# Kernel tuning notes

Hardware: AMD Instinct MI355X
Metric: run time of the kernel (lower is better)

## Reference

```python
import jax, jax.numpy as jnp
import numpy as np

H, D = 8, 16
F = H * D              # hidden_dim = 128
L = 2                  # num HGT layers
NS = [50000, 20000, 10000]                     # gene, disease, drug node counts
EDGE_META = [(0, 0), (0, 1), (2, 0), (2, 1)]   # (src_type, dst_type) per edge type
ES = [300000, 150000, 100000, 50000]
OFFS = [0, NS[0], NS[0] + NS[1], NS[0] + NS[1] + NS[2]]
NTOT = OFFS[-1]
R, T = len(EDGE_META), len(NS)
SQRT_D = float(np.sqrt(D))


def setup_inputs() -> dict:
    key = jax.random.key(0)
    ks = jax.random.split(key, 32)
    inp = {}
    inp["x_gene"] = jax.random.normal(ks[0], (NS[0], F), jnp.float32)
    inp["x_disease"] = jax.random.normal(ks[1], (NS[1], F), jnp.float32)
    inp["x_drug"] = jax.random.normal(ks[2], (NS[2], F), jnp.float32)
    inp["Wkqv"] = 0.05 * jax.random.normal(ks[3], (L, T, F, 3 * F), jnp.float32)
    inp["bkqv"] = jnp.zeros((L, T, 3 * F), jnp.float32)
    inp["Ak"] = 0.1 * jax.random.normal(ks[4], (L, R, H, D, D), jnp.float32)
    inp["Av"] = 0.1 * jax.random.normal(ks[5], (L, R, H, D, D), jnp.float32)
    inp["prel"] = jnp.ones((L, R, H), jnp.float32)   # PyG inits p_rel to ones
    inp["Wout"] = 0.05 * jax.random.normal(ks[6], (L, T, F, F), jnp.float32)
    inp["bout"] = jnp.zeros((L, T, F), jnp.float32)
    inp["skip"] = jnp.ones((L, T), jnp.float32)      # PyG inits skip to 1
    names = ["ei_gg", "ei_gd", "ei_rg", "ei_rd"]
    for i, (name, (st, dt), E) in enumerate(zip(names, EDGE_META, ES)):
        src = jax.random.randint(ks[10 + 2 * i], (E,), 0, NS[st], dtype=jnp.int32)
        dst = jax.random.randint(ks[11 + 2 * i], (E,), 0, NS[dt], dtype=jnp.int32)
        inp[name] = jnp.stack([src, dst])
    return inp


def _hgt_layer(xs, eis, Wkqv_l, bkqv_l, Ak_l, Av_l, prel_l, Wout_l, bout_l, skip_l):
    """One PyG-style HGTConv layer over the heterogeneous graph."""
    kqv = [x @ Wkqv_l[t] + bkqv_l[t] for t, x in enumerate(xs)]
    k = [a[:, :F].reshape(-1, H, D) for a in kqv]
    q = [a[:, F:2 * F].reshape(-1, H, D) for a in kqv]
    v = [a[:, 2 * F:].reshape(-1, H, D) for a in kqv]

    alphas, dsts, ves = [], [], []
    for r, (st, dt) in enumerate(EDGE_META):
        src, dst = eis[r][0], eis[r][1]
        # relation-specific per-head transforms applied on source node set
        k_r = jnp.einsum('nhd,hde->nhe', k[st], Ak_l[r])
        v_r = jnp.einsum('nhd,hde->nhe', v[st], Av_l[r])
        ke = k_r[src]                      # [E, H, D]
        ve = v_r[src]                      # [E, H, D]
        qe = q[dt][dst]                    # [E, H, D]
        a = (qe * ke).sum(-1) * prel_l[r] / SQRT_D   # [E, H]
        alphas.append(a)
        dsts.append(dst + OFFS[dt])
        ves.append(ve)
    alpha = jnp.concatenate(alphas, 0)     # [Etot, H]
    dstg = jnp.concatenate(dsts, 0)        # [Etot]
    ve = jnp.concatenate(ves, 0)           # [Etot, H, D]

    # segment softmax over all incoming edges per destination node
    amax = jax.ops.segment_max(alpha, dstg, num_segments=NTOT)
    ex = jnp.exp(alpha - amax[dstg])
    denom = jax.ops.segment_sum(ex, dstg, num_segments=NTOT)
    w = ex / denom[dstg]
    out = jax.ops.segment_sum(ve * w[..., None], dstg, num_segments=NTOT)
    out = out.reshape(NTOT, F)

    new_xs = []
    for t, x in enumerate(xs):
        o_t = out[OFFS[t]:OFFS[t + 1]]
        o = jax.nn.gelu(o_t, approximate=False) @ Wout_l[t] + bout_l[t]
        a_s = jax.nn.sigmoid(skip_l[t])
        new_xs.append(a_s * o + (1.0 - a_s) * x)
    return new_xs


def reference(x_gene, x_disease, x_drug, Wkqv, bkqv, Ak, Av, prel, Wout, bout,
              skip, ei_gg, ei_gd, ei_rg, ei_rd):
    xs = [x_gene, x_disease, x_drug]
    eis = [ei_gg, ei_gd, ei_rg, ei_rd]
    for l in range(L):
        new = _hgt_layer(xs, eis, Wkqv[l], bkqv[l], Ak[l], Av[l], prel[l],
                         Wout[l], bout[l], skip[l])
        # encoder: dropout(relu(conv_out)) + residual; dropout = identity (eval)
        xs = [jax.nn.relu(n) + x for n, x in zip(new, xs)]
    return tuple(xs)
```

## Files before the change

kernel.cpp:

```cpp
#include <hip/hip_runtime.h>


#define NTOT  80000
#define ETOT  600000
#define NSRC  120000
#define SLOTS 128

typedef unsigned short u16;
typedef unsigned int   u32;
typedef __attribute__((ext_vector_type(8))) short short8;
typedef __attribute__((ext_vector_type(4))) float f32x4;

__device__ __forceinline__ u16 f2bf(float f){
  union { float f; u32 i; } v; v.f = f;
  u32 x = v.i;
  return (u16)((x + 0x7fffu + ((x >> 16) & 1u)) >> 16);
}
__device__ __forceinline__ void unp4(uint4 a, float* o){
  union { u32 i; float f; } t;
  t.i = a.x << 16;        o[0]=t.f;  t.i = a.x & 0xffff0000u; o[1]=t.f;
  t.i = a.y << 16;        o[2]=t.f;  t.i = a.y & 0xffff0000u; o[3]=t.f;
  t.i = a.z << 16;        o[4]=t.f;  t.i = a.z & 0xffff0000u; o[5]=t.f;
  t.i = a.w << 16;        o[6]=t.f;  t.i = a.w & 0xffff0000u; o[7]=t.f;
}
__device__ __forceinline__ void load16bf(const u16* p, float* o){
  unp4(*(const uint4*)p, o); unp4(*(const uint4*)(p + 8), o + 8);
}


#define PR0 2560000
#define PR1 (PR0 + 8*32768)
#define PR2 (PR1 + 2*6*16384)
#define PR3 (PR2 + 2048)
#define PR4 (PR3 + ETOT)

__global__ __launch_bounds__(256) void prep_all(
    const float* __restrict__ xg, const float* __restrict__ xd,
    const float* __restrict__ xr, float* __restrict__ X, u16* __restrict__ Xbf,
    const float* __restrict__ Wkqv, const float* __restrict__ bkqv,
    const float* __restrict__ Ak, const float* __restrict__ Av,
    const float* __restrict__ Wout,
    u16* __restrict__ WeffT, u16* __restrict__ WqT, u16* __restrict__ WoutT,
    float* __restrict__ beff,
    const int* __restrict__ e0, const int* __restrict__ e1,
    const int* __restrict__ e2, const int* __restrict__ e3,
    int* __restrict__ cnt, int* __restrict__ elist)
{
  int i = blockIdx.x * 256 + threadIdx.x;
  if (i < PR0){
    const float* src; int off;
    if (i < 1600000)      { src = xg; off = i; }
    else if (i < 2240000) { src = xd; off = i - 1600000; }
    else                  { src = xr; off = i - 2240000; }
    float4 v = ((const float4*)src)[off];
    ((float4*)X)[i] = v;
    uint2 b;
    b.x = (u32)f2bf(v.x) | ((u32)f2bf(v.y) << 16);
    b.y = (u32)f2bf(v.z) | ((u32)f2bf(v.w) << 16);
    ((uint2*)Xbf)[i] = b;
    return;
  }
  if (i < PR1){
    int j = i - PR0;
    int lr = j >> 15, rem = j & 32767, n = rem >> 7, k = rem & 127;
    int l = lr >> 2, r = lr & 3;
    int st = (r >= 2) ? 2 : 0;
    const float* W = Wkqv + (size_t)(l*3 + st) * 49152;
    float acc = 0.f;
    if (n < 128){
      int h = n >> 4, e = n & 15;
      const float* Am = Ak + (size_t)(l*4 + r) * 2048 + h*256;
#pragma unroll
      for (int d = 0; d < 16; d++) acc += W[k*384 + h*16 + d] * Am[d*16 + e];
    } else {
      int n2 = n - 128, h = n2 >> 4, e = n2 & 15;
      const float* Am = Av + (size_t)(l*4 + r) * 2048 + h*256;
#pragma unroll
      for (int d = 0; d < 16; d++) acc += W[k*384 + 256 + h*16 + d] * Am[d*16 + e];
    }
    WeffT[j] = f2bf(acc);
    return;
  }
  if (i < PR2){
    int j = i - PR1;
    if (j < 6*16384){
      int lt = j >> 14, rem = j & 16383, n = rem >> 7, k = rem & 127;
      WqT[j] = f2bf(Wkqv[(size_t)lt*49152 + k*384 + 128 + n]);
    } else {
      int j2 = j - 6*16384;
      int lt = j2 >> 14, rem = j2 & 16383, n = rem >> 7, k = rem & 127;
      WoutT[j2] = f2bf(Wout[(size_t)lt*16384 + k*128 + n]);
    }
    return;
  }
  if (i < PR3){
    int m = i - PR2;
    int lr = m >> 8, jj = m & 255;
    int l = lr >> 2, r = lr & 3;
    int st = (r >= 2) ? 2 : 0;
    const float* b = bkqv + (size_t)(l*3 + st) * 384;
    float acc = 0.f;
    if (jj < 128){
      int h = jj >> 4, e = jj & 15;
      const float* Am = Ak + (size_t)(l*4 + r) * 2048 + h*256;
#pragma unroll
      for (int d = 0; d < 16; d++) acc += b[h*16 + d] * Am[d*16 + e];
    } else {
      int j2 = jj - 128, h = j2 >> 4, e = j2 & 15;
      const float* Am = Av + (size_t)(l*4 + r) * 2048 + h*256;
#pragma unroll
      for (int d = 0; d < 16; d++) acc += b[256 + h*16 + d] * Am[d*16 + e];
    }
    beff[lr * 256 + jj] = acc;
    return;
  }
  if (i < PR4){
    int e = i - PR3;
    const int* ei; int E, loc, offd, rnoff, rel;
    if (e < 300000)      { ei = e0; E = 300000; loc = e;          offd = 0;     rnoff = 0;      rel = 0; }
    else if (e < 450000) { ei = e1; E = 150000; loc = e - 300000; offd = 50000; rnoff = 50000;  rel = 1; }
    else if (e < 550000) { ei = e2; E = 100000; loc = e - 450000; offd = 0;     rnoff = 100000; rel = 2; }
    else                 { ei = e3; E = 50000;  loc = e - 550000; offd = 50000; rnoff = 110000; rel = 3; }
    int src = ei[loc], dst = ei[E + loc];
    int dstg = offd + dst;
    int pos = atomicAdd(&cnt[dstg], 1);
    if (pos < SLOTS) elist[dstg*SLOTS + pos] = ((rnoff + src) << 2) | rel;
  }
}


__device__ __forceinline__ void stage_bt(const u16* __restrict__ src, u16* BTl){
  int tid = threadIdx.x;
  const uint4* g = (const uint4*)src;
  uint4 tmp[8];
#pragma unroll
  for (int i = 0; i < 8; i++) tmp[i] = g[tid + i*256];
#pragma unroll
  for (int i = 0; i < 8; i++){
    int L = (tid + i*256) * 16;
    int Ls = L ^ (((L >> 8) & 7) << 4);
    *(uint4*)((char*)BTl + Ls) = tmp[i];
  }
}

__device__ __forceinline__ void gemm_core16(
    const u16* __restrict__ A, const u16* BTl, int M, int bm,
    f32x4 acc[8])
{
  int tid = threadIdx.x;
  int lane = tid & 63, w = tid >> 6;
  int quad = lane >> 4, lm = lane & 15;
  int row = bm + w*16 + lm;
  short8 af[4];
  if (row < M){
    const u16* ap = A + (size_t)row*128 + quad*8;
#pragma unroll
    for (int c = 0; c < 4; c++) af[c] = *(const short8*)(ap + c*32);
  } else {
    short8 z = {0,0,0,0,0,0,0,0};
#pragma unroll
    for (int c = 0; c < 4; c++) af[c] = z;
  }
#pragma unroll
  for (int nt = 0; nt < 8; nt++) acc[nt] = (f32x4){0.f,0.f,0.f,0.f};
#pragma unroll
  for (int nt = 0; nt < 8; nt++){
    int rowb = nt*16 + lm;
    int base = rowb*256 + quad*16;
    int sw = (rowb & 7) << 4;
#pragma unroll
    for (int c = 0; c < 4; c++){
      short8 bf = *(const short8*)((const char*)BTl + ((base + c*64) ^ sw));
      acc[nt] = __builtin_amdgcn_mfma_f32_16x16x32_bf16(af[c], bf, acc[nt], 0, 0, 0);
    }
  }
}

__global__ __launch_bounds__(256) void mfma_gemm_qkv(
    const u16* __restrict__ Xbf,
    const u16* __restrict__ WqTl, const float* __restrict__ bl,
    const u16* __restrict__ WeffTl, const float* __restrict__ beffl,
    u16* __restrict__ qg, u16* __restrict__ kv)
{
  __shared__ u16 BTl[16384];
  int by = blockIdx.x;
  const u16* A; const u16* BT; const float* bias;
  u16* C; int ldc, bm, M, bn;
  if (by < 1252){
    int t, roff;
    if (by < 782)       { t = 0; bm = by*64;         M = 50000; roff = 0; }
    else if (by < 1095) { t = 1; bm = (by-782)*64;   M = 20000; roff = 50000; }
    else                { t = 2; bm = (by-1095)*64;  M = 10000; roff = 70000; }
    A = Xbf + (size_t)roff*128;
    BT = WqTl + (size_t)t*16384;
    bias = bl + (size_t)t*384 + 128;
    C = qg + (size_t)roff*128; ldc = 128; bn = 0;
  } else {
    int idx = by - 1252;
    bn = (idx < 1878) ? 0 : 128;
    int tile = (idx < 1878) ? idx : idx - 1878;
    int r, soff, ooff;
    if (tile < 782)       { r = 0; bm = tile*64;        M = 50000; soff = 0;     ooff = 0; }
    else if (tile < 1564) { r = 1; bm = (tile-782)*64;  M = 50000; soff = 0;     ooff = 50000; }
    else if (tile < 1721) { r = 2; bm = (tile-1564)*64; M = 10000; soff = 70000; ooff = 100000; }
    else                  { r = 3; bm = (tile-1721)*64; M = 10000; soff = 70000; ooff = 110000; }
    A = Xbf + (size_t)soff*128;
    BT = WeffTl + (size_t)r*32768 + (size_t)bn*128;
    bias = beffl + (size_t)r*256 + bn;
    C = kv + (size_t)ooff*256 + bn; ldc = 256;
  }
  stage_bt(BT, BTl);
  __syncthreads();
  f32x4 acc[8];
  gemm_core16(A, BTl, M, bm, acc);
  int lane = threadIdx.x & 63, w = threadIdx.x >> 6;
  int quad = lane >> 4, lm = lane & 15;
#pragma unroll
  for (int nt = 0; nt < 8; nt++){
    int col = nt*16 + lm;
    float bb = bias[col];
#pragma unroll
    for (int i = 0; i < 4; i++){
      int r = bm + w*16 + quad*4 + i;
      if (r < M) C[(size_t)r*ldc + col] = f2bf(acc[nt][i] + bb);
    }
  }
}


__global__ __launch_bounds__(256) void attn_out(
    const u16* __restrict__ qg,
    const u16* __restrict__ kv,
    const float* __restrict__ prel,
    const int* __restrict__ cnt,
    const int* __restrict__ elist,
    const u16* __restrict__ WoutTl,
    const float* __restrict__ bl,
    const float* __restrict__ skipl,
    float* __restrict__ Xall, u16* __restrict__ Xbfall)
{
  __shared__ u16 BT[16384];
  __shared__ u16 G[2048];
  int bid = blockIdx.x;
  int t, bm, roff;
  if (bid < 3125)      { t = 0; bm = bid*16;        roff = 0; }
  else if (bid < 4375) { t = 1; bm = (bid-3125)*16; roff = 50000; }
  else                 { t = 2; bm = (bid-4375)*16; roff = 70000; }

  stage_bt(WoutTl + (size_t)t*16384, BT);

  int tid = threadIdx.x;
  int slot = tid >> 4;
  int n = roff + bm + slot;
  int lane = tid & 63;
  int sub = (lane >> 3) & 1;
  int h = lane & 7;
  float sc0 = prel[0*8+h]*0.25f, sc1 = prel[1*8+h]*0.25f,
        sc2 = prel[2*8+h]*0.25f, sc3 = prel[3*8+h]*0.25f;
  float q[16];
  load16bf(qg + (size_t)n * 128 + h*16, q);
  float acc[16] = {};
  float dsum = 0.f;
  int start = n * SLOTS, c = cnt[n];
  if (c > SLOTS) c = SLOTS;

  auto edge = [&](int ev, uint4 ka, uint4 kb, uint4 va, uint4 vb){
    float ke[16], ve[16];
    unp4(ka, ke); unp4(kb, ke + 8);
    unp4(va, ve); unp4(vb, ve + 8);
    float a = 0.f;
#pragma unroll
    for (int d = 0; d < 16; d++) a += q[d] * ke[d];
    int r = ev & 3;
    float s = (r == 0) ? sc0 : (r == 1) ? sc1 : (r == 2) ? sc2 : sc3;
    float ex = expf(a * s);
    dsum += ex;
#pragma unroll
    for (int d = 0; d < 16; d++) acc[d] += ex * ve[d];
  };

  int idx = sub;
#pragma unroll 1
  for (; idx + 6 < c; idx += 8){
    int e0 = elist[start + idx + 0], e1 = elist[start + idx + 2],
        e2 = elist[start + idx + 4], e3 = elist[start + idx + 6];
    const u16* p0 = kv + (size_t)(e0 >> 2) * 256 + h*16;
    const u16* p1 = kv + (size_t)(e1 >> 2) * 256 + h*16;
    const u16* p2 = kv + (size_t)(e2 >> 2) * 256 + h*16;
    const u16* p3 = kv + (size_t)(e3 >> 2) * 256 + h*16;
    uint4 k0a = *(const uint4*)p0,         k0b = *(const uint4*)(p0 + 8);
    uint4 k1a = *(const uint4*)p1,         k1b = *(const uint4*)(p1 + 8);
    uint4 k2a = *(const uint4*)p2,         k2b = *(const uint4*)(p2 + 8);
    uint4 k3a = *(const uint4*)p3,         k3b = *(const uint4*)(p3 + 8);
    uint4 v0a = *(const uint4*)(p0 + 128), v0b = *(const uint4*)(p0 + 136);
    uint4 v1a = *(const uint4*)(p1 + 128), v1b = *(const uint4*)(p1 + 136);
    uint4 v2a = *(const uint4*)(p2 + 128), v2b = *(const uint4*)(p2 + 136);
    uint4 v3a = *(const uint4*)(p3 + 128), v3b = *(const uint4*)(p3 + 136);
    edge(e0, k0a, k0b, v0a, v0b);
    edge(e1, k1a, k1b, v1a, v1b);
    edge(e2, k2a, k2b, v2a, v2b);
    edge(e3, k3a, k3b, v3a, v3b);
  }
#pragma unroll 1
  for (; idx < c; idx += 2){
    int ev = elist[start + idx];
    const u16* p = kv + (size_t)(ev >> 2) * 256 + h*16;
    uint4 ka = *(const uint4*)p,         kb = *(const uint4*)(p + 8);
    uint4 va = *(const uint4*)(p + 128), vb = *(const uint4*)(p + 136);
    edge(ev, ka, kb, va, vb);
  }

  dsum += __shfl_xor(dsum, 8);
#pragma unroll
  for (int d = 0; d < 16; d++) acc[d] += __shfl_xor(acc[d], 8);

  if (sub == 0){
    float inv = (c > 0) ? 1.f / dsum : 0.f;
    u16 o[16];
#pragma unroll
    for (int d = 0; d < 16; d++){
      float x = acc[d] * inv;
      o[d] = f2bf(0.5f * x * (1.f + erff(x * 0.70710678118654752f)));
    }
    uint4 p0, p1;
    p0.x = o[0]|(o[1]<<16);   p0.y = o[2]|(o[3]<<16);
    p0.z = o[4]|(o[5]<<16);   p0.w = o[6]|(o[7]<<16);
    p1.x = o[8]|(o[9]<<16);   p1.y = o[10]|(o[11]<<16);
    p1.z = o[12]|(o[13]<<16); p1.w = o[14]|(o[15]<<16);
    int b0 = slot*256 + h*32;
    int sw = (slot & 7) << 4;
    *(uint4*)((char*)G + (b0 ^ sw))        = p0;
    *(uint4*)((char*)G + ((b0 + 16) ^ sw)) = p1;
  }
  __syncthreads();

  int w = tid >> 6;
  int quad = lane >> 4, lm = lane & 15;
  short8 af[4];
  {
    int base = lm*256 + quad*16;
    int sw = (lm & 7) << 4;
#pragma unroll
    for (int c2 = 0; c2 < 4; c2++)
      af[c2] = *(const short8*)((const char*)G + ((base + c2*64) ^ sw));
  }
  f32x4 oacc[2];
#pragma unroll
  for (int nt = 0; nt < 2; nt++){
    oacc[nt] = (f32x4){0.f,0.f,0.f,0.f};
    int rowb = w*32 + nt*16 + lm;
    int base = rowb*256 + quad*16;
    int sw = (rowb & 7) << 4;
#pragma unroll
    for (int c2 = 0; c2 < 4; c2++){
      short8 bf = *(const short8*)((const char*)BT + ((base + c2*64) ^ sw));
      oacc[nt] = __builtin_amdgcn_mfma_f32_16x16x32_bf16(af[c2], bf, oacc[nt], 0, 0, 0);
    }
  }
  float a_s = 1.f / (1.f + expf(-skipl[t]));
  float b_s = 1.f - a_s;
  const float* bias = bl + (size_t)t*128;
  float* X = Xall + (size_t)roff*128;
  u16* Xb = Xbfall ? (Xbfall + (size_t)roff*128) : (u16*)0;
#pragma unroll
  for (int nt = 0; nt < 2; nt++){
    int col = w*32 + nt*16 + lm;
    float bb = bias[col];
#pragma unroll
    for (int i = 0; i < 4; i++){
      int r = bm + quad*4 + i;
      float* xp = X + (size_t)r*128 + col;
      float x = *xp;
      float o = oacc[nt][i] + bb;
      float xn = fmaxf(a_s*o + b_s*x, 0.f) + x;
      *xp = xn;
      if (Xb) Xb[(size_t)r*128 + col] = f2bf(xn);
    }
  }
}


extern "C" void kernel_launch(void* const* d_in, const int* in_sizes, int n_in,
                              void* d_out, int out_size, void* d_ws, size_t ws_size,
                              hipStream_t stream)
{
  const float* xg   = (const float*)d_in[0];
  const float* xd   = (const float*)d_in[1];
  const float* xr_  = (const float*)d_in[2];
  const float* Wkqv = (const float*)d_in[3];
  const float* bkqv = (const float*)d_in[4];
  const float* Ak   = (const float*)d_in[5];
  const float* Av   = (const float*)d_in[6];
  const float* prel = (const float*)d_in[7];
  const float* Wout = (const float*)d_in[8];
  const float* bout = (const float*)d_in[9];
  const float* skip = (const float*)d_in[10];
  const int* ei[4] = {(const int*)d_in[11], (const int*)d_in[12],
                      (const int*)d_in[13], (const int*)d_in[14]};

  float* X = (float*)d_out;

  char* p = (char*)d_ws;
  auto alloc = [&](size_t b)->void*{ void* r = (void*)p; p += (b + 255) & ~(size_t)255; return r; };
  int*   cnt   = (int*)  alloc((size_t)NTOT * 4);
  int*   elist = (int*)  alloc((size_t)NTOT * SLOTS * 4);
  float* beff  = (float*)alloc((size_t)8 * 256 * 4);
  u16*   qg    = (u16*)  alloc((size_t)NTOT * 128 * 2);
  u16*   kv    = (u16*)  alloc((size_t)NSRC * 256 * 2);
  u16*   Xbf   = (u16*)  alloc((size_t)NTOT * 128 * 2);
  u16*   WqT   = (u16*)  alloc((size_t)6 * 16384 * 2);
  u16*   WeffT = (u16*)  alloc((size_t)8 * 32768 * 2);
  u16*   WoutT = (u16*)  alloc((size_t)6 * 16384 * 2);
  (void)ws_size; (void)in_sizes; (void)n_in; (void)out_size;

  hipMemsetAsync(cnt, 0, (size_t)NTOT * 4, stream);

  prep_all<<<(PR4 + 255)/256, 256, 0, stream>>>(
      xg, xd, xr_, X, Xbf,
      Wkqv, bkqv, Ak, Av, Wout, WeffT, WqT, WoutT, beff,
      ei[0], ei[1], ei[2], ei[3], cnt, elist);

  for (int l = 0; l < 2; l++){
    mfma_gemm_qkv<<<1252 + 3756, 256, 0, stream>>>(
        Xbf,
        WqT + (size_t)l*3*16384, bkqv + (size_t)l*3*384,
        WeffT + (size_t)l*4*32768, beff + (size_t)l*4*256,
        qg, kv);
    attn_out<<<5000, 256, 0, stream>>>(
        qg, kv, prel + l*32, cnt, elist,
        WoutT + (size_t)l*3*16384, bout + (size_t)l*3*128, skip + l*3,
        X, (l == 0) ? Xbf : (u16*)0);
  }
}
```

Measured before the change: 409.6 us.

## Reuse A fragments across Q and KV tiles; load Wout directly into registers

```diff
diff --git a/kernel.cpp b/kernel.cpp
--- a/kernel.cpp
+++ b/kernel.cpp
@@ -143,24 +143,16 @@
   }
 }
 
-__device__ __forceinline__ void gemm_core16(
-    const u16* __restrict__ A, const u16* BTl, int M, int bm,
-    f32x4 acc[8])
+__device__ __forceinline__ void do_tile(
+    const u16* __restrict__ BTsrc, const float* __restrict__ bias,
+    u16* __restrict__ C, int ldc, int bm, int M, const short8 af[4], u16* BTl)
 {
+  stage_bt(BTsrc, BTl);
+  __syncthreads();
   int tid = threadIdx.x;
   int lane = tid & 63, w = tid >> 6;
   int quad = lane >> 4, lm = lane & 15;
-  int row = bm + w*16 + lm;
-  short8 af[4];
-  if (row < M){
-    const u16* ap = A + (size_t)row*128 + quad*8;
-#pragma unroll
-    for (int c = 0; c < 4; c++) af[c] = *(const short8*)(ap + c*32);
-  } else {
-    short8 z = {0,0,0,0,0,0,0,0};
-#pragma unroll
-    for (int c = 0; c < 4; c++) af[c] = z;
-  }
+  f32x4 acc[8];
 #pragma unroll
   for (int nt = 0; nt < 8; nt++) acc[nt] = (f32x4){0.f,0.f,0.f,0.f};
 #pragma unroll
@@ -172,6 +164,17 @@
     for (int c = 0; c < 4; c++){
       short8 bf = *(const short8*)((const char*)BTl + ((base + c*64) ^ sw));
       acc[nt] = __builtin_amdgcn_mfma_f32_16x16x32_bf16(af[c], bf, acc[nt], 0, 0, 0);
+    }
+  }
+  __syncthreads();
+#pragma unroll
+  for (int nt = 0; nt < 8; nt++){
+    int col = nt*16 + lm;
+    float bb = bias[col];
+#pragma unroll
+    for (int i = 0; i < 4; i++){
+      int r = bm + w*16 + quad*4 + i;
+      if (r < M) C[(size_t)r*ldc + col] = f2bf(acc[nt][i] + bb);
     }
   }
 }
@@ -184,45 +187,37 @@
 {
   __shared__ u16 BTl[16384];
   int by = blockIdx.x;
-  const u16* A; const u16* BT; const float* bias;
-  u16* C; int ldc, bm, M, bn;
-  if (by < 1252){
-    int t, roff;
-    if (by < 782)       { t = 0; bm = by*64;         M = 50000; roff = 0; }
-    else if (by < 1095) { t = 1; bm = (by-782)*64;   M = 20000; roff = 50000; }
-    else                { t = 2; bm = (by-1095)*64;  M = 10000; roff = 70000; }
-    A = Xbf + (size_t)roff*128;
-    BT = WqTl + (size_t)t*16384;
-    bias = bl + (size_t)t*384 + 128;
-    C = qg + (size_t)roff*128; ldc = 128; bn = 0;
+  int t, bm, M, roff, rbase, o0, o1; bool haskv;
+  if (by < 782)      { t = 0; bm = by*64;        M = 50000; roff = 0;     haskv = true;  rbase = 0; o0 = 0;      o1 = 50000; }
+  else if (by < 939) { t = 2; bm = (by-782)*64;  M = 10000; roff = 70000; haskv = true;  rbase = 2; o0 = 100000; o1 = 110000; }
+  else               { t = 1; bm = (by-939)*64;  M = 20000; roff = 50000; haskv = false; rbase = 0; o0 = 0;      o1 = 0; }
+
+  int tid = threadIdx.x;
+  int lane = tid & 63, w = tid >> 6;
+  int quad = lane >> 4, lm = lane & 15;
+  int row = bm + w*16 + lm;
+  short8 af[4];
+  if (row < M){
+    const u16* ap = Xbf + (size_t)(roff + row)*128 + quad*8;
+#pragma unroll
+    for (int c = 0; c < 4; c++) af[c] = *(const short8*)(ap + c*32);
   } else {
-    int idx = by - 1252;
-    bn = (idx < 1878) ? 0 : 128;
-    int tile = (idx < 1878) ? idx : idx - 1878;
-    int r, soff, ooff;
-    if (tile < 782)       { r = 0; bm = tile*64;        M = 50000; soff = 0;     ooff = 0; }
-    else if (tile < 1564) { r = 1; bm = (tile-782)*64;  M = 50000; soff = 0;     ooff = 50000; }
-    else if (tile < 1721) { r = 2; bm = (tile-1564)*64; M = 10000; soff = 70000; ooff = 100000; }
-    else                  { r = 3; bm = (tile-1721)*64; M = 10000; soff = 70000; ooff = 110000; }
-    A = Xbf + (size_t)soff*128;
-    BT = WeffTl + (size_t)r*32768 + (size_t)bn*128;
-    bias = beffl + (size_t)r*256 + bn;
-    C = kv + (size_t)ooff*256 + bn; ldc = 256;
-  }
-  stage_bt(BT, BTl);
-  __syncthreads();
-  f32x4 acc[8];
-  gemm_core16(A, BTl, M, bm, acc);
-  int lane = threadIdx.x & 63, w = threadIdx.x >> 6;
-  int quad = lane >> 4, lm = lane & 15;
-#pragma unroll
-  for (int nt = 0; nt < 8; nt++){
-    int col = nt*16 + lm;
-    float bb = bias[col];
-#pragma unroll
-    for (int i = 0; i < 4; i++){
-      int r = bm + w*16 + quad*4 + i;
-      if (r < M) C[(size_t)r*ldc + col] = f2bf(acc[nt][i] + bb);
+    short8 z = {0,0,0,0,0,0,0,0};
+#pragma unroll
+    for (int c = 0; c < 4; c++) af[c] = z;
+  }
+
+  do_tile(WqTl + (size_t)t*16384, bl + (size_t)t*384 + 128,
+          qg + (size_t)roff*128, 128, bm, M, af, BTl);
+  if (haskv){
+#pragma unroll 1
+    for (int s = 0; s < 4; s++){
+      int r  = rbase + (s >> 1);
+      int bn = (s & 1) * 128;
+      int oo = (s < 2) ? o0 : o1;
+      do_tile(WeffTl + (size_t)r*32768 + (size_t)bn*128,
+              beffl + (size_t)r*256 + bn,
+              kv + (size_t)oo*256 + bn, 256, bm, M, af, BTl);
     }
   }
 }
@@ -239,15 +234,12 @@
     const float* __restrict__ skipl,
     float* __restrict__ Xall, u16* __restrict__ Xbfall)
 {
-  __shared__ u16 BT[16384];
   __shared__ u16 G[2048];
   int bid = blockIdx.x;
   int t, bm, roff;
   if (bid < 3125)      { t = 0; bm = bid*16;        roff = 0; }
   else if (bid < 4375) { t = 1; bm = (bid-3125)*16; roff = 50000; }
   else                 { t = 2; bm = (bid-4375)*16; roff = 70000; }
-
-  stage_bt(WoutTl + (size_t)t*16384, BT);
 
   int tid = threadIdx.x;
   int slot = tid >> 4;
@@ -310,6 +302,19 @@
     edge(ev, ka, kb, va, vb);
   }
 
+  int w = tid >> 6;
+  int quad = lane >> 4, lm = lane & 15;
+  short8 wf[2][4];
+  {
+    const u16* wp = WoutTl + (size_t)t*16384;
+#pragma unroll
+    for (int nt = 0; nt < 2; nt++){
+      const u16* wr = wp + (size_t)(w*32 + nt*16 + lm)*128 + quad*8;
+#pragma unroll
+      for (int c2 = 0; c2 < 4; c2++) wf[nt][c2] = *(const short8*)(wr + c2*32);
+    }
+  }
+
   dsum += __shfl_xor(dsum, 8);
 #pragma unroll
   for (int d = 0; d < 16; d++) acc[d] += __shfl_xor(acc[d], 8);
@@ -334,8 +339,6 @@
   }
   __syncthreads();
 
-  int w = tid >> 6;
-  int quad = lane >> 4, lm = lane & 15;
   short8 af[4];
   {
     int base = lm*256 + quad*16;
@@ -348,14 +351,9 @@
 #pragma unroll
   for (int nt = 0; nt < 2; nt++){
     oacc[nt] = (f32x4){0.f,0.f,0.f,0.f};
-    int rowb = w*32 + nt*16 + lm;
-    int base = rowb*256 + quad*16;
-    int sw = (rowb & 7) << 4;
-#pragma unroll
-    for (int c2 = 0; c2 < 4; c2++){
-      short8 bf = *(const short8*)((const char*)BT + ((base + c2*64) ^ sw));
-      oacc[nt] = __builtin_amdgcn_mfma_f32_16x16x32_bf16(af[c2], bf, oacc[nt], 0, 0, 0);
-    }
+#pragma unroll
+    for (int c2 = 0; c2 < 4; c2++)
+      oacc[nt] = __builtin_amdgcn_mfma_f32_16x16x32_bf16(af[c2], wf[nt][c2], oacc[nt], 0, 0, 0);
   }
   float a_s = 1.f / (1.f + expf(-skipl[t]));
   float b_s = 1.f - a_s;
@@ -421,7 +419,7 @@
       ei[0], ei[1], ei[2], ei[3], cnt, elist);
 
   for (int l = 0; l < 2; l++){
-    mfma_gemm_qkv<<<1252 + 3756, 256, 0, stream>>>(
+    mfma_gemm_qkv<<<1252, 256, 0, stream>>>(
         Xbf,
         WqT + (size_t)l*3*16384, bkqv + (size_t)l*3*384,
         WeffT + (size_t)l*4*32768, beff + (size_t)l*4*256,
```

New measurement: 396.4 us. 1.03x faster.
